# Optimization experiments

Measured on AMD Instinct MI355X. Metric: run time of the kernel, lower is better.

## Reference

```python
import jax, jax.numpy as jnp
import numpy as np

DIM = 256
HEADS = 4
HEAD_DIM = DIM // HEADS  # 64
SCALE = (DIM / HEADS) ** -0.5
EPS = 1e-5


def layer_norm(x, g, b):
    mu = jnp.mean(x, axis=-1, keepdims=True)
    var = jnp.mean(jnp.square(x - mu), axis=-1, keepdims=True)
    return (x - mu) * jax.lax.rsqrt(var + EPS) * g + b


def setup_inputs() -> dict:
    key = jax.random.key(0)
    ks = jax.random.split(key, 8)
    B, N, C = 2, 64 * 64, DIM
    H = 4 * DIM  # mlp hidden
    s = lambda fan: 1.0 / np.sqrt(fan)
    return {
        "x": jax.random.normal(ks[0], (B, N, C), jnp.float32),
        "w_qkv": jax.random.normal(ks[1], (C, 3 * C), jnp.float32) * s(C),
        "w_ao": jax.random.normal(ks[2], (C, C), jnp.float32) * s(C),
        "b_ao": jnp.zeros((C,), jnp.float32),
        "g_ao": jnp.ones((C,), jnp.float32),
        "be_ao": jnp.zeros((C,), jnp.float32),
        "g1": jnp.ones((C,), jnp.float32),
        "be1": jnp.zeros((C,), jnp.float32),
        "w_fc1": jax.random.normal(ks[3], (C, H), jnp.float32) * s(C),
        "b_fc1": jnp.zeros((H,), jnp.float32),
        "w_fc2": jax.random.normal(ks[4], (H, C), jnp.float32) * s(H),
        "b_fc2": jnp.zeros((C,), jnp.float32),
        "g2": jnp.ones((C,), jnp.float32),
        "be2": jnp.zeros((C,), jnp.float32),
    }


def reference(x, w_qkv, w_ao, b_ao, g_ao, be_ao, g1, be1,
              w_fc1, b_fc1, w_fc2, b_fc2, g2, be2):
    b, n, c = x.shape
    shortcut = x

    # --- LinearAttention ---
    qkv = x @ w_qkv  # [b, n, 3c]
    qkv = qkv.reshape(b, n, 3, HEADS, HEAD_DIM).transpose(2, 0, 3, 1, 4)  # [3,b,h,n,d]
    q, k, v = qkv[0], qkv[1], qkv[2]
    k = jax.nn.softmax(k, axis=-2)  # softmax over sequence dim
    q = q * SCALE
    context = jnp.einsum('bhid,bhjd->bhij', k, v)   # [b,h,n,n]
    out = jnp.einsum('bhij,bhid->bhjd', context, q)  # [b,h,n,d]
    out = out.reshape(b, n, c)  # faithful to torch reshape (no transpose)
    attn_out = layer_norm(out @ w_ao + b_ao, g_ao, be_ao)

    # --- block residuals ---
    h = shortcut + layer_norm(attn_out, g1, be1)
    mlp = jax.nn.gelu(h @ w_fc1 + b_fc1) @ w_fc2 + b_fc2
    h = h + layer_norm(mlp, g2, be2)
    return shortcut + h
```

## Files before the change

### kernel.cpp

```cpp
#include <hip/hip_runtime.h>

typedef __attribute__((ext_vector_type(8))) short short8;
typedef __attribute__((ext_vector_type(4))) float f32x4;

#define EPSF 1e-5f
#define NSEQ 4096
#define R_TOT 8192

__device__ __forceinline__ float bf2f(unsigned short u){
  union { unsigned int i; float f; } v; v.i = ((unsigned int)u) << 16; return v.f;
}
__device__ __forceinline__ unsigned short f2bf(float f){
  union { float f; unsigned int i; } v; v.f = f;
  unsigned int u = v.i;
  u += 0x7FFFu + ((u >> 16) & 1u);
  return (unsigned short)(u >> 16);
}
__device__ __forceinline__ float wsum(float v){
  #pragma unroll
  for (int o = 32; o > 0; o >>= 1) v += __shfl_xor(v, o, 64);
  return v;
}
__device__ __forceinline__ float gelu_tanh(float x){
  float y = 0.7978845608028654f * (x + 0.044715f * x * x * x);
  float e = __expf(2.0f * y);
  float th = 1.0f - 2.0f / (e + 1.0f);
  return 0.5f * x * (1.0f + th);
}
__device__ __forceinline__ void gload_lds16(const unsigned short* g, unsigned short* l){
  __builtin_amdgcn_global_load_lds(
      (const __attribute__((address_space(1))) unsigned int*)g,
      (__attribute__((address_space(3))) unsigned int*)l, 16, 0, 0);
}

__global__ void k_prep(const float* __restrict__ w_qkv, const float* __restrict__ w_ao,
                       const float* __restrict__ w_fc1, const float* __restrict__ w_fc2,
                       unsigned short* __restrict__ oq, unsigned short* __restrict__ oa,
                       unsigned short* __restrict__ o1, unsigned short* __restrict__ o2)
{
  int bid = blockIdx.x;
  const int t = threadIdx.x;
  const float* in; unsigned short* out; int rows, cols, tid;
  if (bid < 48)      { in = w_qkv; out = oq; rows = 256;  cols = 768;  tid = bid; }
  else if (bid < 64) { in = w_ao;  out = oa; rows = 256;  cols = 256;  tid = bid - 48; }
  else if (bid < 128){ in = w_fc1; out = o1; rows = 256;  cols = 1024; tid = bid - 64; }
  else               { in = w_fc2; out = o2; rows = 1024; cols = 256;  tid = bid - 128; }
  const int tC = cols >> 6;
  const int r0 = (tid / tC) * 64, c0 = (tid % tC) * 64;
  __shared__ float tile[64][68];
  const int i = t >> 4, j4 = (t & 15) * 4;
  #pragma unroll
  for (int p = 0; p < 4; p++){
    float4 v = *(const float4*)(in + (size_t)(r0 + i + p * 16) * cols + c0 + j4);
    tile[i + p * 16][j4 + 0] = v.x; tile[i + p * 16][j4 + 1] = v.y;
    tile[i + p * 16][j4 + 2] = v.z; tile[i + p * 16][j4 + 3] = v.w;
  }
  __syncthreads();
  #pragma unroll
  for (int p = 0; p < 4; p++){
    int ci = i + p * 16;
    ushort4 o;
    o.x = f2bf(tile[j4 + 0][ci]); o.y = f2bf(tile[j4 + 1][ci]);
    o.z = f2bf(tile[j4 + 2][ci]); o.w = f2bf(tile[j4 + 3][ci]);
    *(ushort4*)(out + (size_t)(c0 + ci) * rows + r0 + j4) = o;
  }
}

__global__ __launch_bounds__(256) void k_qkv(const float* __restrict__ X,
                                             const unsigned short* __restrict__ BT,
                                             unsigned short* __restrict__ Cb)
{
  constexpr int K = 256, N = 768;
  __shared__ unsigned short As[2][128 * 72];
  __shared__ unsigned short Bs[2][128 * 64];
  const int t = threadIdx.x, l = t & 63, w = t >> 6;
  const int wm = w >> 1, wn = w & 1, lr = l & 15, kq = l >> 4;
  const int m0 = blockIdx.y * 128, n0 = blockIdx.x * 128;
  const int srow = t >> 1, scol = (t & 1) * 32;
  const int crow = l >> 3, ccolE = (l & 7) * 8;

  f32x4 acc[4][4];
  #pragma unroll
  for (int i = 0; i < 4; i++)
    #pragma unroll
    for (int j = 0; j < 4; j++) acc[i][j] = (f32x4){0.f, 0.f, 0.f, 0.f};

  float4 a4[8];
  auto loadA = [&](int s){
    const float* xp = X + (size_t)(m0 + srow) * K + s * 64 + scol;
    #pragma unroll
    for (int i = 0; i < 8; i++) a4[i] = *(const float4*)(xp + i * 4);
  };
  auto writeA = [&](int bsel){
    unsigned short* d = &As[bsel][srow * 72 + scol];
    #pragma unroll
    for (int i = 0; i < 8; i++){
      ushort4 o;
      o.x = f2bf(a4[i].x); o.y = f2bf(a4[i].y);
      o.z = f2bf(a4[i].z); o.w = f2bf(a4[i].w);
      *(ushort4*)(d + i * 4) = o;
    }
  };
  auto stageB = [&](int s, int bsel){
    #pragma unroll
    for (int c = w; c < 16; c += 4)
      gload_lds16(BT + (size_t)(n0 + c * 8 + crow) * K + s * 64 + ccolE, &Bs[bsel][c * 512]);
  };

  loadA(0); stageB(0, 0); writeA(0);
  __syncthreads();
  for (int s = 0; s < 4; ++s){
    const int cur = s & 1;
    if (s + 1 < 4){ loadA(s + 1); stageB(s + 1, cur ^ 1); }
    #pragma unroll
    for (int kk = 0; kk < 64; kk += 32){
      short8 af[4], bfr[4];
      #pragma unroll
      for (int i = 0; i < 4; i++)
        af[i]  = *(const short8*)&As[cur][(wm * 64 + i * 16 + lr) * 72 + kk + kq * 8];
      #pragma unroll
      for (int j = 0; j < 4; j++)
        bfr[j] = *(const short8*)&Bs[cur][(wn * 64 + j * 16 + lr) * 64 + kk + kq * 8];
      #pragma unroll
      for (int i = 0; i < 4; i++)
        #pragma unroll
        for (int j = 0; j < 4; j++)
          acc[i][j] = __builtin_amdgcn_mfma_f32_16x16x32_bf16(af[i], bfr[j], acc[i][j], 0, 0, 0);
    }
    if (s + 1 < 4) writeA(cur ^ 1);
    __syncthreads();
  }

  const int row0 = m0 + wm * 64;
  const int col0 = n0 + wn * 64;
  #pragma unroll
  for (int i = 0; i < 4; i++)
    #pragma unroll
    for (int j = 0; j < 4; j++)
      #pragma unroll
      for (int r = 0; r < 4; r++){
        int row = row0 + i * 16 + kq * 4 + r;
        int col = col0 + j * 16 + lr;
        Cb[(size_t)row * N + col] = f2bf(acc[i][j][r]);
      }
}

#define NPAD 72
__global__ __launch_bounds__(256) void k_msum(const unsigned short* __restrict__ qkv,
                                              float* __restrict__ Spart,
                                              float* __restrict__ dsum_part)
{
  __shared__ unsigned short kT[64 * NPAD];
  __shared__ unsigned short qT[80 * NPAD];
  const int t = threadIdx.x;
  const int sl = blockIdx.x;
  const int bh = blockIdx.y;
  const int b = bh >> 2, h = bh & 3;
  const int e4 = (t & 15) * 4;
  const int col = (t >> 4) * 4;
  const int w4 = t >> 6, lr = t & 15, kq = (t >> 4) & 3;

  f32x4 acc[5];
  #pragma unroll
  for (int j = 0; j < 5; ++j) acc[j] = (f32x4){0.f, 0.f, 0.f, 0.f};

  for (int ch = 0; ch < 2; ++ch){
    int n = sl * 128 + ch * 64 + col;
    const unsigned short* rp = qkv + (size_t)(b * NSEQ + n) * 768 + h * 64 + e4;
    ushort4 q0 = *(const ushort4*)(rp);
    ushort4 q1 = *(const ushort4*)(rp + 768);
    ushort4 q2 = *(const ushort4*)(rp + 1536);
    ushort4 q3 = *(const ushort4*)(rp + 2304);
    ushort4 k0 = *(const ushort4*)(rp + 256);
    ushort4 k1 = *(const ushort4*)(rp + 1024);
    ushort4 k2 = *(const ushort4*)(rp + 1792);
    ushort4 k3 = *(const ushort4*)(rp + 2560);
    if (ch) __syncthreads();
    ushort4 w;
    w.x = q0.x; w.y = q1.x; w.z = q2.x; w.w = q3.x; *(ushort4*)&qT[(e4+0)*NPAD + col] = w;
    w.x = q0.y; w.y = q1.y; w.z = q2.y; w.w = q3.y; *(ushort4*)&qT[(e4+1)*NPAD + col] = w;
    w.x = q0.z; w.y = q1.z; w.z = q2.z; w.w = q3.z; *(ushort4*)&qT[(e4+2)*NPAD + col] = w;
    w.x = q0.w; w.y = q1.w; w.z = q2.w; w.w = q3.w; *(ushort4*)&qT[(e4+3)*NPAD + col] = w;
    w.x = f2bf(__expf(bf2f(k0.x))); w.y = f2bf(__expf(bf2f(k1.x)));
    w.z = f2bf(__expf(bf2f(k2.x))); w.w = f2bf(__expf(bf2f(k3.x)));
    *(ushort4*)&kT[(e4+0)*NPAD + col] = w;
    w.x = f2bf(__expf(bf2f(k0.y))); w.y = f2bf(__expf(bf2f(k1.y)));
    w.z = f2bf(__expf(bf2f(k2.y))); w.w = f2bf(__expf(bf2f(k3.y)));
    *(ushort4*)&kT[(e4+1)*NPAD + col] = w;
    w.x = f2bf(__expf(bf2f(k0.z))); w.y = f2bf(__expf(bf2f(k1.z)));
    w.z = f2bf(__expf(bf2f(k2.z))); w.w = f2bf(__expf(bf2f(k3.z)));
    *(ushort4*)&kT[(e4+2)*NPAD + col] = w;
    w.x = f2bf(__expf(bf2f(k0.w))); w.y = f2bf(__expf(bf2f(k1.w)));
    w.z = f2bf(__expf(bf2f(k2.w))); w.w = f2bf(__expf(bf2f(k3.w)));
    *(ushort4*)&kT[(e4+3)*NPAD + col] = w;
    if (ch == 0 && t < 16){
      ushort4 ones; ones.x = 0x3F80; ones.y = 0x3F80; ones.z = 0x3F80; ones.w = 0x3F80;
      *(ushort4*)&qT[64 * NPAD + t * 4] = ones;
    }
    __syncthreads();
    #pragma unroll
    for (int ks = 0; ks < 2; ++ks){
      int nc = ks * 32 + kq * 8;
      short8 af = *(const short8*)&kT[(w4 * 16 + lr) * NPAD + nc];
      #pragma unroll
      for (int j = 0; j < 5; ++j){
        short8 bf = *(const short8*)&qT[(j * 16 + lr) * NPAD + nc];
        acc[j] = __builtin_amdgcn_mfma_f32_16x16x32_bf16(af, bf, acc[j], 0, 0, 0);
      }
    }
  }
  float* sp = Spart + ((size_t)sl * 8 + bh) * 4096;
  #pragma unroll
  for (int j = 0; j < 4; ++j)
    #pragma unroll
    for (int r = 0; r < 4; ++r)
      sp[(w4 * 16 + kq * 4 + r) * 64 + j * 16 + lr] = acc[j][r];
  if (lr == 0){
    float* dp = dsum_part + (sl * 8 + bh) * 64;
    #pragma unroll
    for (int r = 0; r < 4; ++r) dp[w4 * 16 + kq * 4 + r] = acc[4][r];
  }
}

__global__ __launch_bounds__(256) void k_projvm_fc1(
    const unsigned short* __restrict__ qkv,
    const float* __restrict__ Spart, const float* __restrict__ dsum_part,
    const unsigned short* __restrict__ waoT,
    const float* __restrict__ bias, const float* __restrict__ x,
    const float* __restrict__ g_ao, const float* __restrict__ be_ao,
    const float* __restrict__ g1, const float* __restrict__ be1,
    const unsigned short* __restrict__ wfc1T, const float* __restrict__ b_fc1,
    float* __restrict__ sxh, unsigned short* __restrict__ mlp1)
{
  __shared__ __align__(16) char smem[140288];
  unsigned short* hA   = (unsigned short*)smem;
  unsigned short* vlds = (unsigned short*)(smem + 16896);
  unsigned short* mt   = (unsigned short*)(smem + 33280);
  unsigned short* Bs0  = (unsigned short*)(smem + 41472);
  float*          yt   = (float*)(smem + 107008);

  const int t = threadIdx.x, l = t & 63, w = t >> 6;
  const int lr = l & 15, kq = l >> 4;
  const int m0 = blockIdx.x * 32;
  const int b = m0 >> 12, h = (m0 >> 10) & 3;
  const int bh = b * 4 + h;
  const int n0 = (m0 & 1023) * 4;
  const int crow = l >> 3, ccolE = (l & 7) * 8;

  const unsigned short* vbase = qkv + (size_t)(b * NSEQ + n0) * 768 + 512 + h * 64;
  #pragma unroll
  for (int c = w; c < 16; c += 4)
    gload_lds16(vbase + (size_t)(c * 8 + crow) * 768 + ccolE, vlds + c * 512);
  #pragma unroll
  for (int c = w; c < 32; c += 4)
    gload_lds16(waoT + (size_t)(c * 8 + crow) * 256 + ccolE, Bs0 + c * 512);
  {
    int e = t >> 2, d0 = (t & 3) * 16;
    float dn = 0.f;
    #pragma unroll 8
    for (int sl = 0; sl < 32; ++sl) dn += dsum_part[(sl * 8 + bh) * 64 + e];
    float rdn = 0.125f / dn;
    #pragma unroll
    for (int i = 0; i < 16; i += 4){
      float4 mv = {0.f, 0.f, 0.f, 0.f};
      #pragma unroll 8
      for (int sl = 0; sl < 32; ++sl){
        float4 p = *(const float4*)(Spart + ((size_t)sl * 8 + bh) * 4096 + e * 64 + d0 + i);
        mv.x += p.x; mv.y += p.y; mv.z += p.z; mv.w += p.w;
      }
      mt[(d0 + i + 0) * 64 + e] = f2bf(mv.x * rdn);
      mt[(d0 + i + 1) * 64 + e] = f2bf(mv.y * rdn);
      mt[(d0 + i + 2) * 64 + e] = f2bf(mv.z * rdn);
      mt[(d0 + i + 3) * 64 + e] = f2bf(mv.w * rdn);
    }
  }
  __syncthreads();
  {
    f32x4 vacc[2][4];
    #pragma unroll
    for (int i = 0; i < 2; i++)
      #pragma unroll
      for (int j = 0; j < 4; j++) vacc[i][j] = (f32x4){0.f, 0.f, 0.f, 0.f};
    #pragma unroll
    for (int kk = 0; kk < 64; kk += 32){
      short8 vf[2], mf[4];
      #pragma unroll
      for (int i = 0; i < 2; i++)
        vf[i] = *(const short8*)&vlds[((w * 2 + i) * 16 + lr) * 64 + kk + kq * 8];
      #pragma unroll
      for (int j = 0; j < 4; j++)
        mf[j] = *(const short8*)&mt[(j * 16 + lr) * 64 + kk + kq * 8];
      #pragma unroll
      for (int i = 0; i < 2; i++)
        #pragma unroll
        for (int j = 0; j < 4; j++)
          vacc[i][j] = __builtin_amdgcn_mfma_f32_16x16x32_bf16(vf[i], mf[j], vacc[i][j], 0, 0, 0);
    }
    #pragma unroll
    for (int i = 0; i < 2; i++)
      #pragma unroll
      for (int j = 0; j < 4; j++)
        #pragma unroll
        for (int r = 0; r < 4; r++)
          hA[((w * 2 + i) * 4 + kq) * 264 + r * 64 + j * 16 + lr] = f2bf(vacc[i][j][r]);
  }
  __syncthreads();
  f32x4 acc[2][4];
  #pragma unroll
  for (int i = 0; i < 2; i++)
    #pragma unroll
    for (int j = 0; j < 4; j++) acc[i][j] = (f32x4){0.f, 0.f, 0.f, 0.f};
  for (int s = 0; s < 4; ++s){
    const int cur = s & 1;
    if (s + 1 < 4){
      unsigned short* bnxt = Bs0 + (cur ^ 1) * 16384;
      #pragma unroll
      for (int c = w; c < 32; c += 4)
        gload_lds16(waoT + (size_t)(c * 8 + crow) * 256 + (s + 1) * 64 + ccolE,
                    bnxt + c * 512);
    }
    const unsigned short* bcur = Bs0 + cur * 16384;
    #pragma unroll
    for (int kk = 0; kk < 64; kk += 32){
      short8 af[2], bfr[4];
      #pragma unroll
      for (int i = 0; i < 2; i++)
        af[i] = *(const short8*)&hA[(i * 16 + lr) * 264 + s * 64 + kk + kq * 8];
      #pragma unroll
      for (int j = 0; j < 4; j++)
        bfr[j] = *(const short8*)&bcur[(w * 64 + j * 16 + lr) * 64 + kk + kq * 8];
      #pragma unroll
      for (int i = 0; i < 2; i++)
        #pragma unroll
        for (int j = 0; j < 4; j++)
          acc[i][j] = __builtin_amdgcn_mfma_f32_16x16x32_bf16(af[i], bfr[j], acc[i][j], 0, 0, 0);
    }
    __syncthreads();
  }
  {
    #pragma unroll
    for (int c = w; c < 32; c += 4)
      gload_lds16(wfc1T + (size_t)(c * 8 + crow) * 256 + ccolE, Bs0 + c * 512);
  }
  #pragma unroll
  for (int i = 0; i < 2; i++)
    #pragma unroll
    for (int j = 0; j < 4; j++){
      float bv = bias[w * 64 + j * 16 + lr];
      #pragma unroll
      for (int r = 0; r < 4; r++)
        yt[(i * 16 + kq * 4 + r) * 260 + w * 64 + j * 16 + lr] = acc[i][j][r] + bv;
    }
  __syncthreads();
  const int gl = t & 63;
  #pragma unroll
  for (int rp = 0; rp < 8; rp++){
    int row = rp * 4 + (t >> 6);
    float4 v = *(const float4*)(yt + row * 260 + gl * 4);
    float mu = wsum(v.x + v.y + v.z + v.w) * 0.00390625f;
    float dx = v.x - mu, dy = v.y - mu, dz = v.z - mu, dw = v.w - mu;
    float rstd = rsqrtf(wsum(dx*dx + dy*dy + dz*dz + dw*dw) * 0.00390625f + EPSF);
    float4 ga = *(const float4*)(g_ao + gl * 4);
    float4 ba = *(const float4*)(be_ao + gl * 4);
    float zx = dx * rstd * ga.x + ba.x, zy = dy * rstd * ga.y + ba.y;
    float zz = dz * rstd * ga.z + ba.z, zw = dw * rstd * ga.w + ba.w;
    float mu2 = wsum(zx + zy + zz + zw) * 0.00390625f;
    float ex = zx - mu2, ey = zy - mu2, ez = zz - mu2, ew = zw - mu2;
    float rstd2 = rsqrtf(wsum(ex*ex + ey*ey + ez*ez + ew*ew) * 0.00390625f + EPSF);
    float4 gb = *(const float4*)(g1 + gl * 4);
    float4 bb = *(const float4*)(be1 + gl * 4);
    size_t off = (size_t)(m0 + row) * 256 + gl * 4;
    float4 xr = *(const float4*)(x + off);
    float hx = xr.x + ex * rstd2 * gb.x + bb.x;
    float hy = xr.y + ey * rstd2 * gb.y + bb.y;
    float hz = xr.z + ez * rstd2 * gb.z + bb.z;
    float hw = xr.w + ew * rstd2 * gb.w + bb.w;
    ushort4 hb; hb.x = f2bf(hx); hb.y = f2bf(hy); hb.z = f2bf(hz); hb.w = f2bf(hw);
    *(ushort4*)&hA[row * 264 + gl * 4] = hb;
    float4 sv = {xr.x + hx, xr.y + hy, xr.z + hz, xr.w + hw};
    *(float4*)(sxh + off) = sv;
  }
  __syncthreads();
  f32x4 acc1[2][4];
  #pragma unroll
  for (int i = 0; i < 2; i++)
    #pragma unroll
    for (int j = 0; j < 4; j++) acc1[i][j] = (f32x4){0.f, 0.f, 0.f, 0.f};
  for (int st = 0; st < 16; ++st){
    const int cur = st & 1;
    if (st + 1 < 16){
      int nch = (st + 1) >> 2, ks = (st + 1) & 3;
      unsigned short* bnxt = Bs0 + (cur ^ 1) * 16384;
      #pragma unroll
      for (int c = w; c < 32; c += 4)
        gload_lds16(wfc1T + (size_t)(nch * 256 + c * 8 + crow) * 256 + ks * 64 + ccolE,
                    bnxt + c * 512);
    }
    const unsigned short* bcur = Bs0 + cur * 16384;
    const int ks = st & 3;
    #pragma unroll
    for (int kk = 0; kk < 64; kk += 32){
      short8 af[2], bfr[4];
      #pragma unroll
      for (int i = 0; i < 2; i++)
        af[i] = *(const short8*)&hA[(i * 16 + lr) * 264 + ks * 64 + kk + kq * 8];
      #pragma unroll
      for (int j = 0; j < 4; j++)
        bfr[j] = *(const short8*)&bcur[(w * 64 + j * 16 + lr) * 64 + kk + kq * 8];
      #pragma unroll
      for (int i = 0; i < 2; i++)
        #pragma unroll
        for (int j = 0; j < 4; j++)
          acc1[i][j] = __builtin_amdgcn_mfma_f32_16x16x32_bf16(af[i], bfr[j], acc1[i][j], 0, 0, 0);
    }
    if (ks == 3){
      const int nch = st >> 2;
      #pragma unroll
      for (int j = 0; j < 4; j++){
        int col = nch * 256 + w * 64 + j * 16 + lr;
        float bv = b_fc1[col];
        #pragma unroll
        for (int i = 0; i < 2; i++){
          #pragma unroll
          for (int r = 0; r < 4; r++){
            int row = m0 + i * 16 + kq * 4 + r;
            mlp1[(size_t)row * 1024 + col] = f2bf(gelu_tanh(acc1[i][j][r] + bv));
          }
          acc1[i][j] = (f32x4){0.f, 0.f, 0.f, 0.f};
        }
      }
    }
    __syncthreads();
  }
}

__global__ __launch_bounds__(256) void k_fc2_ln(
    const unsigned short* __restrict__ A, const unsigned short* __restrict__ BT,
    const float* __restrict__ bias, const float* __restrict__ sxh,
    const float* __restrict__ g2, const float* __restrict__ be2,
    float* __restrict__ out)
{
  constexpr int K = 1024;
  __shared__ __align__(16) char smem[8192 + 65536];
  unsigned short* As0 = (unsigned short*)smem;
  unsigned short* Bs0 = (unsigned short*)(smem + 8192);
  float* yt = (float*)(smem + 8192);
  const int t = threadIdx.x, l = t & 63, w = t >> 6;
  const int lr = l & 15, kq = l >> 4;
  const int m0 = blockIdx.x * 32;
  const int crow = l >> 3, ccolE = (l & 7) * 8;
  f32x4 acc[2][4];
  #pragma unroll
  for (int i = 0; i < 2; i++)
    #pragma unroll
    for (int j = 0; j < 4; j++) acc[i][j] = (f32x4){0.f, 0.f, 0.f, 0.f};

  auto stage = [&](int s, int bsel){
    gload_lds16(A + (size_t)(m0 + w * 8 + crow) * K + s * 64 + ccolE,
                As0 + bsel * 2048 + w * 512);
    unsigned short* bdst = Bs0 + bsel * 16384;
    #pragma unroll
    for (int c = w; c < 32; c += 4)
      gload_lds16(BT + (size_t)(c * 8 + crow) * K + s * 64 + ccolE, bdst + c * 512);
  };

  stage(0, 0);
  __syncthreads();
  for (int s = 0; s < 16; ++s){
    const int cur = s & 1;
    if (s + 1 < 16) stage(s + 1, cur ^ 1);
    const unsigned short* acur = As0 + cur * 2048;
    const unsigned short* bcur = Bs0 + cur * 16384;
    #pragma unroll
    for (int kk = 0; kk < 64; kk += 32){
      short8 af[2], bfr[4];
      #pragma unroll
      for (int i = 0; i < 2; i++)
        af[i] = *(const short8*)&acur[(i * 16 + lr) * 64 + kk + kq * 8];
      #pragma unroll
      for (int j = 0; j < 4; j++)
        bfr[j] = *(const short8*)&bcur[(w * 64 + j * 16 + lr) * 64 + kk + kq * 8];
      #pragma unroll
      for (int i = 0; i < 2; i++)
        #pragma unroll
        for (int j = 0; j < 4; j++)
          acc[i][j] = __builtin_amdgcn_mfma_f32_16x16x32_bf16(af[i], bfr[j], acc[i][j], 0, 0, 0);
    }
    __syncthreads();
  }
  #pragma unroll
  for (int i = 0; i < 2; i++)
    #pragma unroll
    for (int j = 0; j < 4; j++){
      float bv = bias[w * 64 + j * 16 + lr];
      #pragma unroll
      for (int r = 0; r < 4; r++)
        yt[(i * 16 + kq * 4 + r) * 260 + w * 64 + j * 16 + lr] = acc[i][j][r] + bv;
    }
  __syncthreads();
  const int gl = t & 63;
  #pragma unroll
  for (int rp = 0; rp < 8; rp++){
    int row = rp * 4 + (t >> 6);
    float4 v = *(const float4*)(yt + row * 260 + gl * 4);
    float mu = wsum(v.x + v.y + v.z + v.w) * 0.00390625f;
    float dx = v.x - mu, dy = v.y - mu, dz = v.z - mu, dw = v.w - mu;
    float rstd = rsqrtf(wsum(dx*dx + dy*dy + dz*dz + dw*dw) * 0.00390625f + EPSF);
    float4 g = *(const float4*)(g2 + gl * 4);
    float4 be = *(const float4*)(be2 + gl * 4);
    size_t off = (size_t)(m0 + row) * 256 + gl * 4;
    float4 sv = *(const float4*)(sxh + off);
    float4 o;
    o.x = sv.x + dx * rstd * g.x + be.x;
    o.y = sv.y + dy * rstd * g.y + be.y;
    o.z = sv.z + dz * rstd * g.z + be.z;
    o.w = sv.w + dw * rstd * g.w + be.w;
    *(float4*)(out + off) = o;
  }
}

extern "C" void kernel_launch(void* const* d_in, const int* in_sizes, int n_in,
                              void* d_out, int out_size, void* d_ws, size_t ws_size,
                              hipStream_t stream)
{
  const float* x     = (const float*)d_in[0];
  const float* w_qkv = (const float*)d_in[1];
  const float* w_ao  = (const float*)d_in[2];
  const float* b_ao  = (const float*)d_in[3];
  const float* g_ao  = (const float*)d_in[4];
  const float* be_ao = (const float*)d_in[5];
  const float* g1    = (const float*)d_in[6];
  const float* be1   = (const float*)d_in[7];
  const float* w_fc1 = (const float*)d_in[8];
  const float* b_fc1 = (const float*)d_in[9];
  const float* w_fc2 = (const float*)d_in[10];
  const float* b_fc2 = (const float*)d_in[11];
  const float* g2    = (const float*)d_in[12];
  const float* be2   = (const float*)d_in[13];
  float* out = (float*)d_out;
  char* ws = (char*)d_ws;

  unsigned short* qkv   = (unsigned short*)(ws + 0);
  unsigned short* wqkvT = (unsigned short*)(ws + 16777216);
  unsigned short* waoT  = (unsigned short*)(ws + 17170432);
  unsigned short* wfc1T = (unsigned short*)(ws + 17301504);
  unsigned short* wfc2T = (unsigned short*)(ws + 17825792);
  float* Spart = (float*)(ws + 18350080);
  float* dsum_part = (float*)(ws + 22544384);
  float* sxh   = (float*)(ws + 22609920);
  unsigned short* mlp1 = (unsigned short*)(ws + 30998528);

  k_prep<<<192, 256, 0, stream>>>(w_qkv, w_ao, w_fc1, w_fc2,
                                  wqkvT, waoT, wfc1T, wfc2T);

  k_qkv<<<dim3(6, 64), 256, 0, stream>>>(x, wqkvT, qkv);

  k_msum<<<dim3(32, 8), 256, 0, stream>>>(qkv, Spart, dsum_part);

  k_projvm_fc1<<<256, 256, 0, stream>>>(qkv, Spart, dsum_part, waoT, b_ao, x,
                                        g_ao, be_ao, g1, be1, wfc1T, b_fc1,
                                        sxh, mlp1);

  k_fc2_ln<<<256, 256, 0, stream>>>(mlp1, wfc2T, b_fc2, sxh, g2, be2, out);
}
```

Measured before the change: 97.11 us.

## Split fused proj/fc1 kernel, add separate partial-sum reduction and tiled fc1 GEMM

The k/v context partial sums are now computed over 64 slices instead of 32, and a new k_mreduce kernel sums them once into global buffers. Previously each of the 256 projection blocks re-reduced all partials itself. The fused attention-projection + fc1 kernel is split: the projection/LayerNorm kernel writes h in bf16 to global memory, and a standalone 128x128-tiled fc1 GEMM with GELU runs on a 512-block grid. This removes redundant reduction work and the low-parallelism, large-LDS fc1 loop, at the cost of two extra launches and a round trip of h through global memory.

```diff
diff --git a/kernel.cpp b/kernel.cpp
--- a/kernel.cpp
+++ b/kernel.cpp
@@ -158,14 +158,8 @@
   const int b = bh >> 2, h = bh & 3;
   const int e4 = (t & 15) * 4;
   const int col = (t >> 4) * 4;
-  const int w4 = t >> 6, lr = t & 15, kq = (t >> 4) & 3;
-
-  f32x4 acc[5];
-  #pragma unroll
-  for (int j = 0; j < 5; ++j) acc[j] = (f32x4){0.f, 0.f, 0.f, 0.f};
-
-  for (int ch = 0; ch < 2; ++ch){
-    int n = sl * 128 + ch * 64 + col;
+  {
+    int n = sl * 64 + col;
     const unsigned short* rp = qkv + (size_t)(b * NSEQ + n) * 768 + h * 64 + e4;
     ushort4 q0 = *(const ushort4*)(rp);
     ushort4 q1 = *(const ushort4*)(rp + 768);
@@ -175,7 +169,6 @@
     ushort4 k1 = *(const ushort4*)(rp + 1024);
     ushort4 k2 = *(const ushort4*)(rp + 1792);
     ushort4 k3 = *(const ushort4*)(rp + 2560);
-    if (ch) __syncthreads();
     ushort4 w;
     w.x = q0.x; w.y = q1.x; w.z = q2.x; w.w = q3.x; *(ushort4*)&qT[(e4+0)*NPAD + col] = w;
     w.x = q0.y; w.y = q1.y; w.z = q2.y; w.w = q3.y; *(ushort4*)&qT[(e4+1)*NPAD + col] = w;
@@ -193,20 +186,24 @@
     w.x = f2bf(__expf(bf2f(k0.w))); w.y = f2bf(__expf(bf2f(k1.w)));
     w.z = f2bf(__expf(bf2f(k2.w))); w.w = f2bf(__expf(bf2f(k3.w)));
     *(ushort4*)&kT[(e4+3)*NPAD + col] = w;
-    if (ch == 0 && t < 16){
-      ushort4 ones; ones.x = 0x3F80; ones.y = 0x3F80; ones.z = 0x3F80; ones.w = 0x3F80;
-      *(ushort4*)&qT[64 * NPAD + t * 4] = ones;
-    }
-    __syncthreads();
-    #pragma unroll
-    for (int ks = 0; ks < 2; ++ks){
-      int nc = ks * 32 + kq * 8;
-      short8 af = *(const short8*)&kT[(w4 * 16 + lr) * NPAD + nc];
-      #pragma unroll
-      for (int j = 0; j < 5; ++j){
-        short8 bf = *(const short8*)&qT[(j * 16 + lr) * NPAD + nc];
-        acc[j] = __builtin_amdgcn_mfma_f32_16x16x32_bf16(af, bf, acc[j], 0, 0, 0);
-      }
+  }
+  if (t < 16){
+    ushort4 ones; ones.x = 0x3F80; ones.y = 0x3F80; ones.z = 0x3F80; ones.w = 0x3F80;
+    *(ushort4*)&qT[64 * NPAD + t * 4] = ones;
+  }
+  __syncthreads();
+  const int w4 = t >> 6, lr = t & 15, kq = (t >> 4) & 3;
+  f32x4 acc[5];
+  #pragma unroll
+  for (int j = 0; j < 5; ++j) acc[j] = (f32x4){0.f, 0.f, 0.f, 0.f};
+  #pragma unroll
+  for (int ks = 0; ks < 2; ++ks){
+    int nc = ks * 32 + kq * 8;
+    short8 af = *(const short8*)&kT[(w4 * 16 + lr) * NPAD + nc];
+    #pragma unroll
+    for (int j = 0; j < 5; ++j){
+      short8 bf = *(const short8*)&qT[(j * 16 + lr) * NPAD + nc];
+      acc[j] = __builtin_amdgcn_mfma_f32_16x16x32_bf16(af, bf, acc[j], 0, 0, 0);
     }
   }
   float* sp = Spart + ((size_t)sl * 8 + bh) * 4096;
@@ -222,22 +219,39 @@
   }
 }
 
-__global__ __launch_bounds__(256) void k_projvm_fc1(
+__global__ void k_mreduce(const float* __restrict__ Spart, const float* __restrict__ dsum_part,
+                          float* __restrict__ Mm, float* __restrict__ dsumb){
+  int bid = blockIdx.x, t = threadIdx.x;
+  if (bid < 128){
+    int idx = bid * 256 + t;
+    float s = 0.f;
+    #pragma unroll 8
+    for (int sl = 0; sl < 64; ++sl) s += Spart[(size_t)sl * 32768 + idx];
+    Mm[idx] = s;
+  } else {
+    int oi = (bid - 128) * 256 + t;
+    float s = 0.f;
+    #pragma unroll 8
+    for (int sl = 0; sl < 64; ++sl) s += dsum_part[sl * 512 + oi];
+    dsumb[oi] = s;
+  }
+}
+
+__global__ __launch_bounds__(256) void k_projvm_dln(
     const unsigned short* __restrict__ qkv,
-    const float* __restrict__ Spart, const float* __restrict__ dsum_part,
+    const float* __restrict__ Mm, const float* __restrict__ dsumb,
     const unsigned short* __restrict__ waoT,
     const float* __restrict__ bias, const float* __restrict__ x,
     const float* __restrict__ g_ao, const float* __restrict__ be_ao,
     const float* __restrict__ g1, const float* __restrict__ be1,
-    const unsigned short* __restrict__ wfc1T, const float* __restrict__ b_fc1,
-    float* __restrict__ sxh, unsigned short* __restrict__ mlp1)
-{
-  __shared__ __align__(16) char smem[140288];
-  unsigned short* hA   = (unsigned short*)smem;
+    unsigned short* __restrict__ hbf, float* __restrict__ sxh)
+{
+  __shared__ __align__(16) char smem[16896 + 16384 + 8192 + 65536];
+  unsigned short* As   = (unsigned short*)smem;
   unsigned short* vlds = (unsigned short*)(smem + 16896);
-  unsigned short* mt   = (unsigned short*)(smem + 33280);
+  unsigned short* mt   = (unsigned short*)(smem + 16896 + 16384);
   unsigned short* Bs0  = (unsigned short*)(smem + 41472);
-  float*          yt   = (float*)(smem + 107008);
+  float*          yt   = (float*)(smem + 41472);
 
   const int t = threadIdx.x, l = t & 63, w = t >> 6;
   const int lr = l & 15, kq = l >> 4;
@@ -256,18 +270,11 @@
     gload_lds16(waoT + (size_t)(c * 8 + crow) * 256 + ccolE, Bs0 + c * 512);
   {
     int e = t >> 2, d0 = (t & 3) * 16;
-    float dn = 0.f;
-    #pragma unroll 8
-    for (int sl = 0; sl < 32; ++sl) dn += dsum_part[(sl * 8 + bh) * 64 + e];
-    float rdn = 0.125f / dn;
+    float rdn = 0.125f / dsumb[bh * 64 + e];
+    const float* mp = Mm + (size_t)bh * 4096 + e * 64 + d0;
     #pragma unroll
     for (int i = 0; i < 16; i += 4){
-      float4 mv = {0.f, 0.f, 0.f, 0.f};
-      #pragma unroll 8
-      for (int sl = 0; sl < 32; ++sl){
-        float4 p = *(const float4*)(Spart + ((size_t)sl * 8 + bh) * 4096 + e * 64 + d0 + i);
-        mv.x += p.x; mv.y += p.y; mv.z += p.z; mv.w += p.w;
-      }
+      float4 mv = *(const float4*)(mp + i);
       mt[(d0 + i + 0) * 64 + e] = f2bf(mv.x * rdn);
       mt[(d0 + i + 1) * 64 + e] = f2bf(mv.y * rdn);
       mt[(d0 + i + 2) * 64 + e] = f2bf(mv.z * rdn);
@@ -302,7 +309,7 @@
       for (int j = 0; j < 4; j++)
         #pragma unroll
         for (int r = 0; r < 4; r++)
-          hA[((w * 2 + i) * 4 + kq) * 264 + r * 64 + j * 16 + lr] = f2bf(vacc[i][j][r]);
+          As[((w * 2 + i) * 4 + kq) * 264 + r * 64 + j * 16 + lr] = f2bf(vacc[i][j][r]);
   }
   __syncthreads();
   f32x4 acc[2][4];
@@ -325,7 +332,7 @@
       short8 af[2], bfr[4];
       #pragma unroll
       for (int i = 0; i < 2; i++)
-        af[i] = *(const short8*)&hA[(i * 16 + lr) * 264 + s * 64 + kk + kq * 8];
+        af[i] = *(const short8*)&As[(i * 16 + lr) * 264 + s * 64 + kk + kq * 8];
       #pragma unroll
       for (int j = 0; j < 4; j++)
         bfr[j] = *(const short8*)&bcur[(w * 64 + j * 16 + lr) * 64 + kk + kq * 8];
@@ -336,11 +343,6 @@
           acc[i][j] = __builtin_amdgcn_mfma_f32_16x16x32_bf16(af[i], bfr[j], acc[i][j], 0, 0, 0);
     }
     __syncthreads();
-  }
-  {
-    #pragma unroll
-    for (int c = w; c < 32; c += 4)
-      gload_lds16(wfc1T + (size_t)(c * 8 + crow) * 256 + ccolE, Bs0 + c * 512);
   }
   #pragma unroll
   for (int i = 0; i < 2; i++)
@@ -376,62 +378,81 @@
     float hz = xr.z + ez * rstd2 * gb.z + bb.z;
     float hw = xr.w + ew * rstd2 * gb.w + bb.w;
     ushort4 hb; hb.x = f2bf(hx); hb.y = f2bf(hy); hb.z = f2bf(hz); hb.w = f2bf(hw);
-    *(ushort4*)&hA[row * 264 + gl * 4] = hb;
+    *(ushort4*)(hbf + off) = hb;
     float4 sv = {xr.x + hx, xr.y + hy, xr.z + hz, xr.w + hw};
     *(float4*)(sxh + off) = sv;
   }
-  __syncthreads();
-  f32x4 acc1[2][4];
-  #pragma unroll
-  for (int i = 0; i < 2; i++)
-    #pragma unroll
-    for (int j = 0; j < 4; j++) acc1[i][j] = (f32x4){0.f, 0.f, 0.f, 0.f};
-  for (int st = 0; st < 16; ++st){
-    const int cur = st & 1;
-    if (st + 1 < 16){
-      int nch = (st + 1) >> 2, ks = (st + 1) & 3;
-      unsigned short* bnxt = Bs0 + (cur ^ 1) * 16384;
-      #pragma unroll
-      for (int c = w; c < 32; c += 4)
-        gload_lds16(wfc1T + (size_t)(nch * 256 + c * 8 + crow) * 256 + ks * 64 + ccolE,
-                    bnxt + c * 512);
-    }
-    const unsigned short* bcur = Bs0 + cur * 16384;
-    const int ks = st & 3;
+}
+
+__global__ __launch_bounds__(256) void k_fc1(const unsigned short* __restrict__ A,
+                       const unsigned short* __restrict__ BT,
+                       const float* __restrict__ bias,
+                       unsigned short* __restrict__ Cb)
+{
+  constexpr int K = 256, N = 1024;
+  __shared__ unsigned short As[2][128 * 64];
+  __shared__ unsigned short Bs[2][128 * 64];
+  const int t  = threadIdx.x;
+  const int l  = t & 63;
+  const int w  = t >> 6;
+  const int wm = w >> 1, wn = w & 1;
+  const int lr = l & 15, kq = l >> 4;
+  const int m0 = blockIdx.y * 128, n0 = blockIdx.x * 128;
+
+  f32x4 acc[4][4];
+  #pragma unroll
+  for (int i = 0; i < 4; i++)
+    #pragma unroll
+    for (int j = 0; j < 4; j++) acc[i][j] = (f32x4){0.f, 0.f, 0.f, 0.f};
+
+  const int crow = l >> 3, ccolE = (l & 7) * 8;
+
+  auto stage = [&](int s, int bsel){
+    #pragma unroll
+    for (int c = w; c < 16; c += 4)
+      gload_lds16(A  + (size_t)(m0 + c * 8 + crow) * K + s * 64 + ccolE, &As[bsel][c * 512]);
+    #pragma unroll
+    for (int c = w; c < 16; c += 4)
+      gload_lds16(BT + (size_t)(n0 + c * 8 + crow) * K + s * 64 + ccolE, &Bs[bsel][c * 512]);
+  };
+
+  stage(0, 0);
+  __syncthreads();
+  for (int s = 0; s < 4; ++s){
+    const int cur = s & 1;
+    if (s + 1 < 4) stage(s + 1, cur ^ 1);
     #pragma unroll
     for (int kk = 0; kk < 64; kk += 32){
-      short8 af[2], bfr[4];
-      #pragma unroll
-      for (int i = 0; i < 2; i++)
-        af[i] = *(const short8*)&hA[(i * 16 + lr) * 264 + ks * 64 + kk + kq * 8];
+      short8 af[4], bfr[4];
+      #pragma unroll
+      for (int i = 0; i < 4; i++)
+        af[i]  = *(const short8*)&As[cur][(wm * 64 + i * 16 + lr) * 64 + kk + kq * 8];
       #pragma unroll
       for (int j = 0; j < 4; j++)
-        bfr[j] = *(const short8*)&bcur[(w * 64 + j * 16 + lr) * 64 + kk + kq * 8];
-      #pragma unroll
-      for (int i = 0; i < 2; i++)
+        bfr[j] = *(const short8*)&Bs[cur][(wn * 64 + j * 16 + lr) * 64 + kk + kq * 8];
+      #pragma unroll
+      for (int i = 0; i < 4; i++)
         #pragma unroll
         for (int j = 0; j < 4; j++)
-          acc1[i][j] = __builtin_amdgcn_mfma_f32_16x16x32_bf16(af[i], bfr[j], acc1[i][j], 0, 0, 0);
-    }
-    if (ks == 3){
-      const int nch = st >> 2;
-      #pragma unroll
-      for (int j = 0; j < 4; j++){
-        int col = nch * 256 + w * 64 + j * 16 + lr;
-        float bv = b_fc1[col];
-        #pragma unroll
-        for (int i = 0; i < 2; i++){
-          #pragma unroll
-          for (int r = 0; r < 4; r++){
-            int row = m0 + i * 16 + kq * 4 + r;
-            mlp1[(size_t)row * 1024 + col] = f2bf(gelu_tanh(acc1[i][j][r] + bv));
-          }
-          acc1[i][j] = (f32x4){0.f, 0.f, 0.f, 0.f};
-        }
+          acc[i][j] = __builtin_amdgcn_mfma_f32_16x16x32_bf16(af[i], bfr[j], acc[i][j], 0, 0, 0);
+    }
+    __syncthreads();
+  }
+
+  const int row0 = m0 + wm * 64;
+  const int col0 = n0 + wn * 64;
+  #pragma unroll
+  for (int i = 0; i < 4; i++)
+    #pragma unroll
+    for (int j = 0; j < 4; j++){
+      float bv = bias[col0 + j * 16 + lr];
+      #pragma unroll
+      for (int r = 0; r < 4; r++){
+        int row = row0 + i * 16 + kq * 4 + r;
+        int col = col0 + j * 16 + lr;
+        Cb[(size_t)row * N + col] = f2bf(gelu_tanh(acc[i][j][r] + bv));
       }
     }
-    __syncthreads();
-  }
 }
 
 __global__ __launch_bounds__(256) void k_fc2_ln(
@@ -541,25 +562,30 @@
   char* ws = (char*)d_ws;
 
   unsigned short* qkv   = (unsigned short*)(ws + 0);
+  unsigned short* hbf   = (unsigned short*)(ws + 12582912);
   unsigned short* wqkvT = (unsigned short*)(ws + 16777216);
   unsigned short* waoT  = (unsigned short*)(ws + 17170432);
   unsigned short* wfc1T = (unsigned short*)(ws + 17301504);
   unsigned short* wfc2T = (unsigned short*)(ws + 17825792);
   float* Spart = (float*)(ws + 18350080);
-  float* dsum_part = (float*)(ws + 22544384);
-  float* sxh   = (float*)(ws + 22609920);
-  unsigned short* mlp1 = (unsigned short*)(ws + 30998528);
+  float* dsum_part = (float*)(ws + 26738688);
+  float* Mm    = (float*)(ws + 26869760);
+  float* dsumb = (float*)(ws + 27000832);
+  float* sxh   = (float*)(ws + 27004928);
+  unsigned short* mlp1 = (unsigned short*)(ws + 35393536);
 
   k_prep<<<192, 256, 0, stream>>>(w_qkv, w_ao, w_fc1, w_fc2,
                                   wqkvT, waoT, wfc1T, wfc2T);
 
   k_qkv<<<dim3(6, 64), 256, 0, stream>>>(x, wqkvT, qkv);
 
-  k_msum<<<dim3(32, 8), 256, 0, stream>>>(qkv, Spart, dsum_part);
-
-  k_projvm_fc1<<<256, 256, 0, stream>>>(qkv, Spart, dsum_part, waoT, b_ao, x,
-                                        g_ao, be_ao, g1, be1, wfc1T, b_fc1,
-                                        sxh, mlp1);
+  k_msum<<<dim3(64, 8), 256, 0, stream>>>(qkv, Spart, dsum_part);
+  k_mreduce<<<130, 256, 0, stream>>>(Spart, dsum_part, Mm, dsumb);
+
+  k_projvm_dln<<<256, 256, 0, stream>>>(qkv, Mm, dsumb, waoT, b_ao, x,
+                                        g_ao, be_ao, g1, be1, hbf, sxh);
+
+  k_fc1<<<dim3(8, 64), 256, 0, stream>>>(hbf, wfc1T, b_fc1, mlp1);
 
   k_fc2_ln<<<256, 256, 0, stream>>>(mlp1, wfc2T, b_fc2, sxh, g2, be2, out);
 }
```

Measured after the change: 81.53 us. 1.19x faster.
